# Kernel optimization log

Measured on AMD Instinct MI355X. Metric: run time of the kernel, lower is better.

## Reference

```python
import jax, jax.numpy as jnp
import numpy as np

N_NODES = 50000
E_EDGES = 800000
NEG_SLOPE = 0.2  # PyG GATConv LeakyReLU slope
BN_EPS = 1e-5


def _gat(x, src, dst, W, a_s, a_d, b, heads, ch, concat):
    """One GATConv (PyG semantics, eval mode): gather, per-edge attention,
    segment softmax over destination neighborhoods, scatter-add aggregation."""
    n = x.shape[0]
    h = (x @ W).reshape(n, heads, ch)                      # [N,H,C]
    es = jnp.sum(h * a_s, axis=-1)                         # [N,H] alpha_src per node
    ed = jnp.sum(h * a_d, axis=-1)                         # [N,H] alpha_dst per node
    e = jax.nn.leaky_relu(es[src] + ed[dst], NEG_SLOPE)    # [E,H] edge logits
    m = jax.ops.segment_max(e, dst, num_segments=n)        # stable segment softmax
    ex = jnp.exp(e - m[dst])
    den = jax.ops.segment_sum(ex, dst, num_segments=n)
    alpha = ex / den[dst]                                  # [E,H]
    out = jax.ops.segment_sum(h[src] * alpha[:, :, None], dst, num_segments=n)  # [N,H,C]
    out = out.reshape(n, heads * ch) if concat else out.mean(axis=1)
    return out + b


def _bn(x, g, b):
    # eval-mode BatchNorm1d with running_mean=0, running_var=1
    return x * (g / jnp.sqrt(1.0 + BN_EPS)) + b


def setup_inputs() -> dict:
    key = jax.random.key(0)
    k = jax.random.split(key, 24)
    s = 0.1
    inp = {
        "x": jax.random.normal(k[0], (N_NODES, 9), jnp.float32),
        "edge_index": jax.random.randint(k[1], (2, E_EDGES), 0, N_NODES, jnp.int32),
        "W1": jax.random.normal(k[2], (9, 512), jnp.float32) * s,
        "a1s": jax.random.normal(k[3], (8, 64), jnp.float32) * s,
        "a1d": jax.random.normal(k[4], (8, 64), jnp.float32) * s,
        "b1": jax.random.normal(k[5], (512,), jnp.float32) * s,
        "W2": jax.random.normal(k[6], (512, 128), jnp.float32) * s,
        "a2s": jax.random.normal(k[7], (4, 32), jnp.float32) * s,
        "a2d": jax.random.normal(k[8], (4, 32), jnp.float32) * s,
        "b2": jax.random.normal(k[9], (128,), jnp.float32) * s,
        "W3": jax.random.normal(k[10], (128, 32), jnp.float32) * s,
        "a3s": jax.random.normal(k[11], (1, 32), jnp.float32) * s,
        "a3d": jax.random.normal(k[12], (1, 32), jnp.float32) * s,
        "b3": jax.random.normal(k[13], (32,), jnp.float32) * s,
        "g1": jax.random.uniform(k[14], (512,), jnp.float32, 0.5, 1.5),
        "be1": jax.random.normal(k[15], (512,), jnp.float32) * s,
        "g2": jax.random.uniform(k[16], (128,), jnp.float32, 0.5, 1.5),
        "be2": jax.random.normal(k[17], (128,), jnp.float32) * s,
        "g3": jax.random.uniform(k[18], (32,), jnp.float32, 0.5, 1.5),
        "be3": jax.random.normal(k[19], (32,), jnp.float32) * s,
        "Wh": jax.random.normal(k[20], (32, 1), jnp.float32) * s,
        "bh": jax.random.normal(k[21], (1,), jnp.float32) * s,
    }
    return inp


def reference(x, edge_index, W1, a1s, a1d, b1, W2, a2s, a2d, b2,
              W3, a3s, a3d, b3, g1, be1, g2, be2, g3, be3, Wh, bh):
    n = x.shape[0]
    loops = jnp.arange(n, dtype=edge_index.dtype)          # PyG add_self_loops=True
    src = jnp.concatenate([edge_index[0], loops])
    dst = jnp.concatenate([edge_index[1], loops])
    h = _gat(x, src, dst, W1, a1s, a1d, b1, heads=8, ch=64, concat=True)
    h = jax.nn.elu(_bn(h, g1, be1))
    h = _gat(h, src, dst, W2, a2s, a2d, b2, heads=4, ch=32, concat=True)
    h = jax.nn.elu(_bn(h, g2, be2))
    h = _gat(h, src, dst, W3, a3s, a3d, b3, heads=1, ch=32, concat=False)
    h = jax.nn.elu(_bn(h, g3, be3))
    return h @ Wh + bh                                     # [N,1]
```

## Files before the change

### kernel.cpp

```cpp
#include <hip/hip_runtime.h>
#include <hip/hip_bf16.h>
#include <math.h>

#define N_NODES 50000
#define E_EDGES 800000
#define ET (E_EDGES + N_NODES)
#define NBLK_SCAN ((N_NODES + 255) / 256)
#define MPAD 50048
#define NPB_T1 16

typedef __attribute__((ext_vector_type(8))) short bf16x8;
typedef __attribute__((ext_vector_type(4))) float f32x4;


__global__ void zero_int_kernel(int* __restrict__ p, int n) {
    int i = blockIdx.x * blockDim.x + threadIdx.x;
    if (i < n) p[i] = 0;
}

__global__ void hist_kernel(const int* __restrict__ ei, int* __restrict__ cnt) {
    int e = blockIdx.x * blockDim.x + threadIdx.x;
    if (e < ET) {
        int d = (e < E_EDGES) ? ei[E_EDGES + e] : (e - E_EDGES);
        atomicAdd(&cnt[d], 1);
    }
}

__global__ void scan1_kernel(const int* __restrict__ cnt, int* __restrict__ rp,
                             int* __restrict__ bsum) {
    __shared__ int s[256];
    int i = blockIdx.x * 256 + threadIdx.x;
    int v = (i < N_NODES) ? cnt[i] : 0;
    s[threadIdx.x] = v;
    __syncthreads();
    for (int off = 1; off < 256; off <<= 1) {
        int t = (threadIdx.x >= off) ? s[threadIdx.x - off] : 0;
        __syncthreads();
        s[threadIdx.x] += t;
        __syncthreads();
    }
    if (i < N_NODES) rp[i + 1] = s[threadIdx.x];
    if (threadIdx.x == 255) bsum[blockIdx.x] = s[255];
}

__global__ void scan2_kernel(int* __restrict__ bsum, int nb) {
    __shared__ int s[256];
    int v = (threadIdx.x < nb) ? bsum[threadIdx.x] : 0;
    s[threadIdx.x] = v;
    __syncthreads();
    for (int off = 1; off < 256; off <<= 1) {
        int t = (threadIdx.x >= off) ? s[threadIdx.x - off] : 0;
        __syncthreads();
        s[threadIdx.x] += t;
        __syncthreads();
    }
    if (threadIdx.x < nb) bsum[threadIdx.x] = (threadIdx.x == 0) ? 0 : s[threadIdx.x - 1];
}

__global__ void scan3_kernel(int* __restrict__ rp, const int* __restrict__ bsum,
                             int* __restrict__ cursor) {
    int i = blockIdx.x * 256 + threadIdx.x;
    if (i == 0) rp[0] = 0;
    if (i < N_NODES) {
        int incl = rp[i + 1] + bsum[i >> 8];
        rp[i + 1] = incl;
        cursor[i] = incl - cursor[i];
    }
}

__global__ void fill_kernel(const int* __restrict__ ei, int* __restrict__ cursor,
                            int* __restrict__ col) {
    int e = blockIdx.x * blockDim.x + threadIdx.x;
    if (e < ET) {
        int s_, d;
        if (e < E_EDGES) { s_ = ei[e]; d = ei[E_EDGES + e]; }
        else             { s_ = e - E_EDGES; d = s_; }
        int p = atomicAdd(&cursor[d], 1);
        col[p] = s_;
    }
}


__global__ void prep_attn1_kernel(const float* __restrict__ W1,
                                  const float* __restrict__ a1s,
                                  const float* __restrict__ a1d,
                                  float* __restrict__ M) {
    int t = threadIdx.x;
    if (t < 144) {
        int which = t / 72, idx = t % 72, k = idx / 8, h = idx % 8;
        const float* a = which ? a1d : a1s;
        float s = 0.f;
        for (int c = 0; c < 64; c++) s += W1[k * 512 + h * 64 + c] * a[h * 64 + c];
        M[t] = s;
    }
}

__global__ void es_ed1_kernel(const float* __restrict__ x, const float* __restrict__ M,
                              float* __restrict__ es, float* __restrict__ ed) {
    int n = blockIdx.x * blockDim.x + threadIdx.x;
    if (n >= N_NODES) return;
    float xr[9];
#pragma unroll
    for (int k = 0; k < 9; k++) xr[k] = x[(size_t)n * 9 + k];
#pragma unroll
    for (int h = 0; h < 8; h++) {
        float s1 = 0.f, s2 = 0.f;
#pragma unroll
        for (int k = 0; k < 9; k++) {
            s1 += xr[k] * M[k * 8 + h];
            s2 += xr[k] * M[72 + k * 8 + h];
        }
        es[(size_t)n * 8 + h] = s1;
        ed[(size_t)n * 8 + h] = s2;
    }
}

__global__ __launch_bounds__(128) void agg1_kernel(const float* __restrict__ x,
        const int* __restrict__ rp, const int* __restrict__ col,
        const float* __restrict__ es, const float* __restrict__ ed,
        float* __restrict__ aggx) {
    __shared__ int   s_src[64];
    __shared__ float s_x[64][9];
    __shared__ float s_es[64][8];
    __shared__ float s_w[8][64];
    __shared__ float s_m[8], s_den[8], s_scale[8], s_ed[8];
    int n = blockIdx.x, tid = threadIdx.x;
    int start = rp[n], end = rp[n + 1];
    if (tid < 8) { s_m[tid] = -INFINITY; s_den[tid] = 0.f; s_ed[tid] = ed[(size_t)n * 8 + tid]; }
    __syncthreads();
    float acc = 0.f;
    int ghh = tid >> 4, glane = tid & 15;
    for (int cs = start; cs < end; cs += 64) {
        int cnt = min(64, end - cs);
        if (tid < cnt) s_src[tid] = col[cs + tid];
        __syncthreads();
        for (int q = tid; q < cnt * 9; q += 128) {
            int e = q / 9, k = q - e * 9;
            s_x[e][k] = x[(size_t)s_src[e] * 9 + k];
        }
        for (int q = tid; q < cnt * 8; q += 128) {
            int e = q >> 3, h = q & 7;
            s_es[e][h] = es[(size_t)s_src[e] * 8 + h];
        }
        __syncthreads();
        float lmax = -INFINITY;
        for (int e = glane; e < cnt; e += 16) {
            float l = s_es[e][ghh] + s_ed[ghh];
            l = (l > 0.f) ? l : 0.2f * l;
            s_w[ghh][e] = l;
            lmax = fmaxf(lmax, l);
        }
#pragma unroll
        for (int off = 8; off > 0; off >>= 1) lmax = fmaxf(lmax, __shfl_xor(lmax, off));
        float mold = s_m[ghh];
        float nm = fmaxf(mold, lmax);
        float fac = __expf(mold - nm);
        float psum = 0.f;
        for (int e = glane; e < cnt; e += 16) {
            float w = __expf(s_w[ghh][e] - nm);
            s_w[ghh][e] = w;
            psum += w;
        }
#pragma unroll
        for (int off = 8; off > 0; off >>= 1) psum += __shfl_xor(psum, off);
        if (glane == 0) { s_den[ghh] = s_den[ghh] * fac + psum; s_m[ghh] = nm; s_scale[ghh] = fac; }
        __syncthreads();
        if (tid < 72) {
            int hh = tid / 9, k = tid - hh * 9;
            float a = acc * s_scale[hh];
            for (int e = 0; e < cnt; e++) a += s_w[hh][e] * s_x[e][k];
            acc = a;
        }
        __syncthreads();
    }
    if (tid < 72) {
        int hh = tid / 9;
        aggx[(size_t)n * 72 + tid] = acc / s_den[hh];
    }
}

__global__ __launch_bounds__(256) void transform1_kernel(const float* __restrict__ aggx,
        const float* __restrict__ W1, const float* __restrict__ b1,
        const float* __restrict__ g1, const float* __restrict__ be1,
        __hip_bfloat16* __restrict__ Ah, __hip_bfloat16* __restrict__ Al) {
    __shared__ float s_a[NPB_T1 * 72];
    int tid = threadIdx.x;
    int n0 = blockIdx.x * NPB_T1;
    int nn = min(NPB_T1, N_NODES - n0);
    for (int q = tid; q < nn * 72; q += 256) s_a[q] = aggx[(size_t)n0 * 72 + q];
    int c0 = tid * 2;
    int hh = c0 >> 6;
    float2 wv[9];
#pragma unroll
    for (int k = 0; k < 9; k++) wv[k] = *(const float2*)&W1[k * 512 + c0];
    float2 bv = *(const float2*)&b1[c0];
    float2 gv = *(const float2*)&g1[c0];
    float2 ev = *(const float2*)&be1[c0];
    float gs0 = gv.x / sqrtf(1.00001f), gs1 = gv.y / sqrtf(1.00001f);
    __syncthreads();
    for (int i = 0; i < nn; i++) {
        const float* ar = &s_a[i * 72 + hh * 9];
        float v0 = bv.x, v1 = bv.y;
#pragma unroll
        for (int k = 0; k < 9; k++) { float a = ar[k]; v0 += a * wv[k].x; v1 += a * wv[k].y; }
        v0 = v0 * gs0 + ev.x;
        v1 = v1 * gs1 + ev.y;
        v0 = (v0 > 0.f) ? v0 : expm1f(v0);
        v1 = (v1 > 0.f) ? v1 : expm1f(v1);
        __hip_bfloat16 h0 = __float2bfloat16(v0), h1 = __float2bfloat16(v1);
        float r0 = v0 - __bfloat162float(h0), r1 = v1 - __bfloat162float(h1);
        size_t base = (size_t)(n0 + i) * 512 + c0;
        __hip_bfloat162 hp; hp.x = h0; hp.y = h1;
        __hip_bfloat162 lp; lp.x = __float2bfloat16(r0); lp.y = __float2bfloat16(r1);
        *(__hip_bfloat162*)&Ah[base] = hp;
        *(__hip_bfloat162*)&Al[base] = lp;
    }
}

__global__ void prep_w2_kernel(const float* __restrict__ W2,
                               __hip_bfloat16* __restrict__ Wh,
                               __hip_bfloat16* __restrict__ Wl) {
    int t = blockIdx.x * 256 + threadIdx.x;
    if (t < 512 * 128) {
        int k = t >> 7, c = t & 127;
        float v = W2[t];
        __hip_bfloat16 hi = __float2bfloat16(v);
        float r = v - __bfloat162float(hi);
        Wh[c * 512 + k] = hi;
        Wl[c * 512 + k] = __float2bfloat16(r);
    }
}


__global__ __launch_bounds__(256) void gemm2_mfma_kernel(
        const __hip_bfloat16* __restrict__ Ah, const __hip_bfloat16* __restrict__ Al,
        const __hip_bfloat16* __restrict__ Wh, const __hip_bfloat16* __restrict__ Wl,
        float* __restrict__ C) {
    __shared__ short lds[32768];
    int tid = threadIdx.x;
    int wv = tid >> 6;
    int lane = tid & 63;
    int lrow = lane & 15, kgrp = lane >> 4;
    int m0 = blockIdx.x * 128;

    f32x4 acc[2][8];
#pragma unroll
    for (int m = 0; m < 2; m++)
#pragma unroll
        for (int n = 0; n < 8; n++) acc[m][n] = (f32x4){0.f, 0.f, 0.f, 0.f};

    for (int kk = 0; kk < 512; kk += 64) {
#pragma unroll
        for (int tI = 0; tI < 4; tI++) {
            const __hip_bfloat16* src = (tI == 0) ? Ah : (tI == 1) ? Al : (tI == 2) ? Wh : Wl;
            int rowBase = (tI < 2) ? m0 : 0;
#pragma unroll
            for (int i = 0; i < 4; i++) {
                int gid = tid + 256 * i;
                int row = gid >> 3, kg = gid & 7;
                bf16x8 v = *(const bf16x8*)(src + (size_t)(rowBase + row) * 512 + kk + kg * 8);
                *(bf16x8*)(lds + tI * 8192 + row * 64 + ((kg ^ (row & 7)) << 3)) = v;
            }
        }
        __syncthreads();
#pragma unroll
        for (int ks = 0; ks < 2; ks++) {
            bf16x8 ah[2], al[2];
#pragma unroll
            for (int m = 0; m < 2; m++) {
                int row = wv * 32 + m * 16 + lrow;
                int kg = ks * 4 + kgrp;
                int so = row * 64 + ((kg ^ (row & 7)) << 3);
                ah[m] = *(const bf16x8*)(lds + so);
                al[m] = *(const bf16x8*)(lds + 8192 + so);
            }
#pragma unroll
            for (int n = 0; n < 8; n++) {
                int colr = n * 16 + lrow;
                int kg = ks * 4 + kgrp;
                int so = colr * 64 + ((kg ^ (colr & 7)) << 3);
                bf16x8 wh = *(const bf16x8*)(lds + 16384 + so);
                bf16x8 wl = *(const bf16x8*)(lds + 24576 + so);
#pragma unroll
                for (int m = 0; m < 2; m++) {
                    acc[m][n] = __builtin_amdgcn_mfma_f32_16x16x32_bf16(ah[m], wh, acc[m][n], 0, 0, 0);
                    acc[m][n] = __builtin_amdgcn_mfma_f32_16x16x32_bf16(al[m], wh, acc[m][n], 0, 0, 0);
                    acc[m][n] = __builtin_amdgcn_mfma_f32_16x16x32_bf16(ah[m], wl, acc[m][n], 0, 0, 0);
                }
            }
        }
        __syncthreads();
    }
#pragma unroll
    for (int m = 0; m < 2; m++) {
#pragma unroll
        for (int n = 0; n < 8; n++) {
#pragma unroll
            for (int r = 0; r < 4; r++) {
                int row = m0 + wv * 32 + m * 16 + (lane >> 4) * 4 + r;
                int colc = n * 16 + (lane & 15);
                if (row < N_NODES) C[(size_t)row * 128 + colc] = acc[m][n][r];
            }
        }
    }
}


template <int TN>
__global__ __launch_bounds__(256) void gemm_kernel(
        const float* __restrict__ A, const float* __restrict__ B,
        float* __restrict__ C, int M, int K, int Nd) {
    constexpr int BM = 64, BK = 16;
    constexpr int BN = 32 * TN;
    __shared__ float As[BM * BK];
    __shared__ float Bs[BK * BN];
    int tid = threadIdx.x;
    int m0 = blockIdx.x * BM;
    int n0 = blockIdx.y * BN;
    int tc = tid & 31;
    int tr = tid >> 5;
    float acc[8][TN];
#pragma unroll
    for (int i = 0; i < 8; i++)
#pragma unroll
        for (int j = 0; j < TN; j++) acc[i][j] = 0.f;

    for (int kk = 0; kk < K; kk += BK) {
#pragma unroll
        for (int l = 0; l < (BM * BK) / 256; l++) {
            int e = tid + 256 * l;
            int r = e >> 4, k = e & 15;
            float v = 0.f;
            if (m0 + r < M && kk + k < K) v = A[(size_t)(m0 + r) * K + kk + k];
            As[e] = v;
        }
#pragma unroll
        for (int l = 0; l < (BK * BN) / 256; l++) {
            int e = tid + 256 * l;
            int r = e / BN, c = e % BN;
            float v = 0.f;
            if (kk + r < K) v = B[(size_t)(kk + r) * Nd + n0 + c];
            Bs[e] = v;
        }
        __syncthreads();
#pragma unroll
        for (int k = 0; k < BK; k++) {
            float bv[TN];
#pragma unroll
            for (int j = 0; j < TN; j++) bv[j] = Bs[k * BN + tc * TN + j];
#pragma unroll
            for (int i = 0; i < 8; i++) {
                float a = As[(tr * 8 + i) * BK + k];
#pragma unroll
                for (int j = 0; j < TN; j++) acc[i][j] += a * bv[j];
            }
        }
        __syncthreads();
    }
#pragma unroll
    for (int i = 0; i < 8; i++) {
        int r = m0 + tr * 8 + i;
        if (r < M) {
#pragma unroll
            for (int j = 0; j < TN; j++)
                C[(size_t)r * Nd + n0 + tc * TN + j] = acc[i][j];
        }
    }
}


template <int H, int C>
__global__ void attn_dots_kernel(const float* __restrict__ hin,
                                 const float* __restrict__ as_, const float* __restrict__ ad_,
                                 float* __restrict__ es, float* __restrict__ ed) {
    int t = blockIdx.x * blockDim.x + threadIdx.x;
    if (t >= N_NODES * H) return;
    int n = t / H, hh = t % H;
    const float* row = hin + (size_t)n * (H * C) + hh * C;
    float s1 = 0.f, s2 = 0.f;
    for (int c = 0; c < C; c++) {
        float v = row[c];
        s1 += v * as_[hh * C + c];
        s2 += v * ad_[hh * C + c];
    }
    es[t] = s1;
    ed[t] = s2;
}


template <int H, int C>
__global__ __launch_bounds__((H * C < 64) ? 64 : H * C) void gat_agg_kernel(
        const float* __restrict__ hin,
        const int* __restrict__ rp, const int* __restrict__ col,
        const float* __restrict__ es, const float* __restrict__ ed,
        const float* __restrict__ bias, const float* __restrict__ gg,
        const float* __restrict__ bb,
        float* __restrict__ out) {
    constexpr int HC  = H * C;
    constexpr int BLK = (HC < 64) ? 64 : HC;
    constexpr int LPH = (BLK / H > 64) ? 64 : (BLK / H);
    constexpr int RT  = HC / 4;
    constexpr int G   = BLK / RT;
    constexpr int CH  = 64;
    __shared__ int   s_src[CH];
    __shared__ float s_w[H][CH];
    __shared__ float s_red[G][HC];
    __shared__ float s_m[H], s_den[H], s_scale[H], s_ed[H];

    int n = blockIdx.x;
    int tid = threadIdx.x;
    int start = rp[n], end = rp[n + 1];
    if (tid < H) {
        s_m[tid] = -INFINITY;
        s_den[tid] = 0.f;
        s_ed[tid] = ed[(size_t)n * H + tid];
    }
    __syncthreads();

    int ghh = tid / LPH, glane = tid % LPH;
    int g = tid / RT, rl = tid % RT;
    int hh2 = (rl * 4) / C;
    float ax = 0.f, ay = 0.f, az = 0.f, aw = 0.f;

    for (int cs = start; cs < end; cs += CH) {
        int cnt = min(CH, end - cs);
        if (tid < cnt) s_src[tid] = col[cs + tid];
        __syncthreads();

        {
            float lmax = -INFINITY;
            for (int e = glane; e < cnt; e += LPH) {
                float l = es[(size_t)s_src[e] * H + ghh] + s_ed[ghh];
                l = (l > 0.f) ? l : 0.2f * l;
                s_w[ghh][e] = l;
                lmax = fmaxf(lmax, l);
            }
#pragma unroll
            for (int off = LPH >> 1; off > 0; off >>= 1)
                lmax = fmaxf(lmax, __shfl_xor(lmax, off));
            float mold = s_m[ghh];
            float nm = fmaxf(mold, lmax);
            float fac = __expf(mold - nm);
            float psum = 0.f;
            for (int e = glane; e < cnt; e += LPH) {
                float w = __expf(s_w[ghh][e] - nm);
                s_w[ghh][e] = w;
                psum += w;
            }
#pragma unroll
            for (int off = LPH >> 1; off > 0; off >>= 1)
                psum += __shfl_xor(psum, off);
            if (glane == 0) {
                s_den[ghh] = s_den[ghh] * fac + psum;
                s_m[ghh] = nm;
                s_scale[ghh] = fac;
            }
        }
        __syncthreads();

        {
            float fac = s_scale[hh2];
            float bx = ax * fac, by = ay * fac, bz = az * fac, bw = aw * fac;
            float cx = 0.f, cy = 0.f, cz = 0.f, cw = 0.f;
            int e = g;
            for (; e + G < cnt; e += 2 * G) {
                float w0 = s_w[hh2][e];
                float w1 = s_w[hh2][e + G];
                float4 v0 = *(const float4*)&hin[(size_t)s_src[e] * HC + rl * 4];
                float4 v1 = *(const float4*)&hin[(size_t)s_src[e + G] * HC + rl * 4];
                bx += w0 * v0.x; by += w0 * v0.y; bz += w0 * v0.z; bw += w0 * v0.w;
                cx += w1 * v1.x; cy += w1 * v1.y; cz += w1 * v1.z; cw += w1 * v1.w;
            }
            if (e < cnt) {
                float w0 = s_w[hh2][e];
                float4 v0 = *(const float4*)&hin[(size_t)s_src[e] * HC + rl * 4];
                bx += w0 * v0.x; by += w0 * v0.y; bz += w0 * v0.z; bw += w0 * v0.w;
            }
            ax = bx + cx; ay = by + cy; az = bz + cz; aw = bw + cw;
        }
        __syncthreads();
    }

    s_red[g][rl * 4 + 0] = ax;
    s_red[g][rl * 4 + 1] = ay;
    s_red[g][rl * 4 + 2] = az;
    s_red[g][rl * 4 + 3] = aw;
    __syncthreads();
    if (tid < HC) {
        int hh = tid / C;
        float res = 0.f;
#pragma unroll
        for (int q = 0; q < G; q++) res += s_red[q][tid];
        res /= s_den[hh];
        res += bias[tid];
        res = res * (gg[tid] / sqrtf(1.00001f)) + bb[tid];
        res = (res > 0.f) ? res : expm1f(res);
        out[(size_t)n * HC + tid] = res;
    }
}


__global__ void head_kernel(const float* __restrict__ h3, const float* __restrict__ Wh,
                            const float* __restrict__ bh, float* __restrict__ out) {
    int n = blockIdx.x * blockDim.x + threadIdx.x;
    if (n < N_NODES) {
        float s = bh[0];
        const float* row = h3 + (size_t)n * 32;
#pragma unroll
        for (int c = 0; c < 32; c++) s += row[c] * Wh[c];
        out[n] = s;
    }
}


extern "C" void kernel_launch(void* const* d_in, const int* in_sizes, int n_in,
                              void* d_out, int out_size, void* d_ws, size_t ws_size,
                              hipStream_t stream) {
    const float* x   = (const float*)d_in[0];
    const int*   ei  = (const int*)d_in[1];
    const float* W1  = (const float*)d_in[2];
    const float* a1s = (const float*)d_in[3];
    const float* a1d = (const float*)d_in[4];
    const float* b1  = (const float*)d_in[5];
    const float* W2  = (const float*)d_in[6];
    const float* a2s = (const float*)d_in[7];
    const float* a2d = (const float*)d_in[8];
    const float* b2  = (const float*)d_in[9];
    const float* W3  = (const float*)d_in[10];
    const float* a3s = (const float*)d_in[11];
    const float* a3d = (const float*)d_in[12];
    const float* b3  = (const float*)d_in[13];
    const float* g1  = (const float*)d_in[14];
    const float* be1 = (const float*)d_in[15];
    const float* g2  = (const float*)d_in[16];
    const float* be2 = (const float*)d_in[17];
    const float* g3  = (const float*)d_in[18];
    const float* be3 = (const float*)d_in[19];
    const float* Wh  = (const float*)d_in[20];
    const float* bh  = (const float*)d_in[21];
    float* out = (float*)d_out;

    char* ws = (char*)d_ws;
    size_t off = 0;
    auto alloc = [&](size_t bytes) -> void* {
        void* p = ws + off;
        off += (bytes + 255) & ~(size_t)255;
        return p;
    };
    int*   row_ptr = (int*)alloc((N_NODES + 1) * sizeof(int));
    int*   cursor  = (int*)alloc((N_NODES + 1) * sizeof(int));
    int*   bsum    = (int*)alloc(256 * sizeof(int));
    int*   col_src = (int*)alloc((size_t)ET * sizeof(int));
    float* es      = (float*)alloc((size_t)N_NODES * 8 * sizeof(float));
    float* ed      = (float*)alloc((size_t)N_NODES * 8 * sizeof(float));
    float* bufA    = (float*)alloc((size_t)N_NODES * 128 * sizeof(float));
    float* bufB    = (float*)alloc((size_t)N_NODES * 128 * sizeof(float));
    float* bufC    = (float*)alloc((size_t)N_NODES * 32 * sizeof(float));
    __hip_bfloat16* Ah   = (__hip_bfloat16*)alloc((size_t)MPAD * 512 * sizeof(__hip_bfloat16));
    __hip_bfloat16* Al   = (__hip_bfloat16*)alloc((size_t)MPAD * 512 * sizeof(__hip_bfloat16));
    __hip_bfloat16* W2Th = (__hip_bfloat16*)alloc((size_t)128 * 512 * sizeof(__hip_bfloat16));
    __hip_bfloat16* W2Tl = (__hip_bfloat16*)alloc((size_t)128 * 512 * sizeof(__hip_bfloat16));
    float* M1 = (float*)(ws + ((ws_size - 1024) & ~(size_t)255));
    float* aggx = bufA;

    zero_int_kernel<<<(N_NODES + 1 + 255) / 256, 256, 0, stream>>>(cursor, N_NODES + 1);
    hist_kernel<<<(ET + 255) / 256, 256, 0, stream>>>(ei, cursor);
    scan1_kernel<<<NBLK_SCAN, 256, 0, stream>>>(cursor, row_ptr, bsum);
    scan2_kernel<<<1, 256, 0, stream>>>(bsum, NBLK_SCAN);
    scan3_kernel<<<NBLK_SCAN, 256, 0, stream>>>(row_ptr, bsum, cursor);
    fill_kernel<<<(ET + 255) / 256, 256, 0, stream>>>(ei, cursor, col_src);

    prep_attn1_kernel<<<1, 256, 0, stream>>>(W1, a1s, a1d, M1);
    es_ed1_kernel<<<(N_NODES + 255) / 256, 256, 0, stream>>>(x, M1, es, ed);
    agg1_kernel<<<N_NODES, 128, 0, stream>>>(x, row_ptr, col_src, es, ed, aggx);
    transform1_kernel<<<(N_NODES + NPB_T1 - 1) / NPB_T1, 256, 0, stream>>>(aggx, W1, b1, g1, be1, Ah, Al);

    prep_w2_kernel<<<256, 256, 0, stream>>>(W2, W2Th, W2Tl);
    gemm2_mfma_kernel<<<MPAD / 128, 256, 0, stream>>>(Ah, Al, W2Th, W2Tl, bufA);
    attn_dots_kernel<4, 32><<<(N_NODES * 4 + 255) / 256, 256, 0, stream>>>(bufA, a2s, a2d, es, ed);
    gat_agg_kernel<4, 32><<<N_NODES, 128, 0, stream>>>(bufA, row_ptr, col_src, es, ed,
                                                       b2, g2, be2, bufB);

    gemm_kernel<1><<<dim3((N_NODES + 63) / 64, 1), 256, 0, stream>>>(bufB, W3, bufC, N_NODES, 128, 32);
    attn_dots_kernel<1, 32><<<(N_NODES + 255) / 256, 256, 0, stream>>>(bufC, a3s, a3d, es, ed);
    gat_agg_kernel<1, 32><<<N_NODES, 64, 0, stream>>>(bufC, row_ptr, col_src, es, ed,
                                                      b3, g3, be3, bufA);

    head_kernel<<<(N_NODES + 255) / 256, 256, 0, stream>>>(bufA, Wh, bh, out);
}
```

Before: 457.4 us.

## Store layer 2 and 3 node features in fp16 to halve gather traffic

Result: faster. 431.8 us (-5.6%).

```diff
diff --git a/kernel.cpp b/kernel.cpp
--- a/kernel.cpp
+++ b/kernel.cpp
@@ -11,6 +11,7 @@
 
 typedef __attribute__((ext_vector_type(8))) short bf16x8;
 typedef __attribute__((ext_vector_type(4))) float f32x4;
+typedef __attribute__((ext_vector_type(8))) _Float16 half8;
 
 
 __global__ void zero_int_kernel(int* __restrict__ p, int n) {
@@ -235,7 +236,7 @@
 __global__ __launch_bounds__(256) void gemm2_mfma_kernel(
         const __hip_bfloat16* __restrict__ Ah, const __hip_bfloat16* __restrict__ Al,
         const __hip_bfloat16* __restrict__ Wh, const __hip_bfloat16* __restrict__ Wl,
-        float* __restrict__ C) {
+        _Float16* __restrict__ C) {
     __shared__ short lds[32768];
     int tid = threadIdx.x;
     int wv = tid >> 6;
@@ -299,7 +300,7 @@
             for (int r = 0; r < 4; r++) {
                 int row = m0 + wv * 32 + m * 16 + (lane >> 4) * 4 + r;
                 int colc = n * 16 + (lane & 15);
-                if (row < N_NODES) C[(size_t)row * 128 + colc] = acc[m][n][r];
+                if (row < N_NODES) C[(size_t)row * 128 + colc] = (_Float16)acc[m][n][r];
             }
         }
     }
@@ -307,9 +308,9 @@
 
 
 template <int TN>
-__global__ __launch_bounds__(256) void gemm_kernel(
+__global__ __launch_bounds__(256) void gemm_h_kernel(
         const float* __restrict__ A, const float* __restrict__ B,
-        float* __restrict__ C, int M, int K, int Nd) {
+        _Float16* __restrict__ C, int M, int K, int Nd) {
     constexpr int BM = 64, BK = 16;
     constexpr int BN = 32 * TN;
     __shared__ float As[BM * BK];
@@ -363,25 +364,30 @@
         if (r < M) {
 #pragma unroll
             for (int j = 0; j < TN; j++)
-                C[(size_t)r * Nd + n0 + tc * TN + j] = acc[i][j];
+                C[(size_t)r * Nd + n0 + tc * TN + j] = (_Float16)acc[i][j];
         }
     }
 }
 
 
 template <int H, int C>
-__global__ void attn_dots_kernel(const float* __restrict__ hin,
-                                 const float* __restrict__ as_, const float* __restrict__ ad_,
-                                 float* __restrict__ es, float* __restrict__ ed) {
+__global__ void attn_dots_h_kernel(const _Float16* __restrict__ hin,
+                                   const float* __restrict__ as_, const float* __restrict__ ad_,
+                                   float* __restrict__ es, float* __restrict__ ed) {
     int t = blockIdx.x * blockDim.x + threadIdx.x;
     if (t >= N_NODES * H) return;
     int n = t / H, hh = t % H;
-    const float* row = hin + (size_t)n * (H * C) + hh * C;
+    const half8* row = (const half8*)(hin + (size_t)n * (H * C) + hh * C);
     float s1 = 0.f, s2 = 0.f;
-    for (int c = 0; c < C; c++) {
-        float v = row[c];
-        s1 += v * as_[hh * C + c];
-        s2 += v * ad_[hh * C + c];
+#pragma unroll
+    for (int c8 = 0; c8 < C / 8; c8++) {
+        half8 v = row[c8];
+#pragma unroll
+        for (int j = 0; j < 8; j++) {
+            float f = (float)v[j];
+            s1 += f * as_[hh * C + c8 * 8 + j];
+            s2 += f * ad_[hh * C + c8 * 8 + j];
+        }
     }
     es[t] = s1;
     ed[t] = s2;
@@ -389,8 +395,8 @@
 
 
 template <int H, int C>
-__global__ __launch_bounds__((H * C < 64) ? 64 : H * C) void gat_agg_kernel(
-        const float* __restrict__ hin,
+__global__ __launch_bounds__((H * C < 64) ? 64 : H * C) void gat_agg_h_kernel(
+        const _Float16* __restrict__ hin,
         const int* __restrict__ rp, const int* __restrict__ col,
         const float* __restrict__ es, const float* __restrict__ ed,
         const float* __restrict__ bias, const float* __restrict__ gg,
@@ -399,7 +405,7 @@
     constexpr int HC  = H * C;
     constexpr int BLK = (HC < 64) ? 64 : HC;
     constexpr int LPH = (BLK / H > 64) ? 64 : (BLK / H);
-    constexpr int RT  = HC / 4;
+    constexpr int RT  = HC / 8;
     constexpr int G   = BLK / RT;
     constexpr int CH  = 64;
     __shared__ int   s_src[CH];
@@ -419,8 +425,10 @@
 
     int ghh = tid / LPH, glane = tid % LPH;
     int g = tid / RT, rl = tid % RT;
-    int hh2 = (rl * 4) / C;
-    float ax = 0.f, ay = 0.f, az = 0.f, aw = 0.f;
+    int hh2 = (rl * 8) / C;
+    float a0[8], a1[8];
+#pragma unroll
+    for (int j = 0; j < 8; j++) { a0[j] = 0.f; a1[j] = 0.f; }
 
     for (int cs = start; cs < end; cs += CH) {
         int cnt = min(CH, end - cs);
@@ -460,31 +468,31 @@
 
         {
             float fac = s_scale[hh2];
-            float bx = ax * fac, by = ay * fac, bz = az * fac, bw = aw * fac;
-            float cx = 0.f, cy = 0.f, cz = 0.f, cw = 0.f;
+#pragma unroll
+            for (int j = 0; j < 8; j++) a0[j] *= fac;
             int e = g;
             for (; e + G < cnt; e += 2 * G) {
                 float w0 = s_w[hh2][e];
                 float w1 = s_w[hh2][e + G];
-                float4 v0 = *(const float4*)&hin[(size_t)s_src[e] * HC + rl * 4];
-                float4 v1 = *(const float4*)&hin[(size_t)s_src[e + G] * HC + rl * 4];
-                bx += w0 * v0.x; by += w0 * v0.y; bz += w0 * v0.z; bw += w0 * v0.w;
-                cx += w1 * v1.x; cy += w1 * v1.y; cz += w1 * v1.z; cw += w1 * v1.w;
+                half8 v0 = *(const half8*)&hin[(size_t)s_src[e] * HC + rl * 8];
+                half8 v1 = *(const half8*)&hin[(size_t)s_src[e + G] * HC + rl * 8];
+#pragma unroll
+                for (int j = 0; j < 8; j++) a0[j] += w0 * (float)v0[j];
+#pragma unroll
+                for (int j = 0; j < 8; j++) a1[j] += w1 * (float)v1[j];
             }
             if (e < cnt) {
                 float w0 = s_w[hh2][e];
-                float4 v0 = *(const float4*)&hin[(size_t)s_src[e] * HC + rl * 4];
-                bx += w0 * v0.x; by += w0 * v0.y; bz += w0 * v0.z; bw += w0 * v0.w;
-            }
-            ax = bx + cx; ay = by + cy; az = bz + cz; aw = bw + cw;
-        }
-        __syncthreads();
-    }
-
-    s_red[g][rl * 4 + 0] = ax;
-    s_red[g][rl * 4 + 1] = ay;
-    s_red[g][rl * 4 + 2] = az;
-    s_red[g][rl * 4 + 3] = aw;
+                half8 v0 = *(const half8*)&hin[(size_t)s_src[e] * HC + rl * 8];
+#pragma unroll
+                for (int j = 0; j < 8; j++) a0[j] += w0 * (float)v0[j];
+            }
+        }
+        __syncthreads();
+    }
+
+#pragma unroll
+    for (int j = 0; j < 8; j++) s_red[g][rl * 8 + j] = a0[j] + a1[j];
     __syncthreads();
     if (tid < HC) {
         int hh = tid / C;
@@ -555,7 +563,8 @@
     float* ed      = (float*)alloc((size_t)N_NODES * 8 * sizeof(float));
     float* bufA    = (float*)alloc((size_t)N_NODES * 128 * sizeof(float));
     float* bufB    = (float*)alloc((size_t)N_NODES * 128 * sizeof(float));
-    float* bufC    = (float*)alloc((size_t)N_NODES * 32 * sizeof(float));
+    _Float16* h2h  = (_Float16*)alloc((size_t)N_NODES * 128 * sizeof(_Float16));
+    _Float16* h3h  = (_Float16*)alloc((size_t)N_NODES * 32 * sizeof(_Float16));
     __hip_bfloat16* Ah   = (__hip_bfloat16*)alloc((size_t)MPAD * 512 * sizeof(__hip_bfloat16));
     __hip_bfloat16* Al   = (__hip_bfloat16*)alloc((size_t)MPAD * 512 * sizeof(__hip_bfloat16));
     __hip_bfloat16* W2Th = (__hip_bfloat16*)alloc((size_t)128 * 512 * sizeof(__hip_bfloat16));
@@ -576,15 +585,15 @@
     transform1_kernel<<<(N_NODES + NPB_T1 - 1) / NPB_T1, 256, 0, stream>>>(aggx, W1, b1, g1, be1, Ah, Al);
 
     prep_w2_kernel<<<256, 256, 0, stream>>>(W2, W2Th, W2Tl);
-    gemm2_mfma_kernel<<<MPAD / 128, 256, 0, stream>>>(Ah, Al, W2Th, W2Tl, bufA);
-    attn_dots_kernel<4, 32><<<(N_NODES * 4 + 255) / 256, 256, 0, stream>>>(bufA, a2s, a2d, es, ed);
-    gat_agg_kernel<4, 32><<<N_NODES, 128, 0, stream>>>(bufA, row_ptr, col_src, es, ed,
-                                                       b2, g2, be2, bufB);
-
-    gemm_kernel<1><<<dim3((N_NODES + 63) / 64, 1), 256, 0, stream>>>(bufB, W3, bufC, N_NODES, 128, 32);
-    attn_dots_kernel<1, 32><<<(N_NODES + 255) / 256, 256, 0, stream>>>(bufC, a3s, a3d, es, ed);
-    gat_agg_kernel<1, 32><<<N_NODES, 64, 0, stream>>>(bufC, row_ptr, col_src, es, ed,
-                                                      b3, g3, be3, bufA);
+    gemm2_mfma_kernel<<<MPAD / 128, 256, 0, stream>>>(Ah, Al, W2Th, W2Tl, h2h);
+    attn_dots_h_kernel<4, 32><<<(N_NODES * 4 + 255) / 256, 256, 0, stream>>>(h2h, a2s, a2d, es, ed);
+    gat_agg_h_kernel<4, 32><<<N_NODES, 128, 0, stream>>>(h2h, row_ptr, col_src, es, ed,
+                                                         b2, g2, be2, bufB);
+
+    gemm_h_kernel<1><<<dim3((N_NODES + 63) / 64, 1), 256, 0, stream>>>(bufB, W3, h3h, N_NODES, 128, 32);
+    attn_dots_h_kernel<1, 32><<<(N_NODES + 255) / 256, 256, 0, stream>>>(h3h, a3s, a3d, es, ed);
+    gat_agg_h_kernel<1, 32><<<N_NODES, 64, 0, stream>>>(h3h, row_ptr, col_src, es, ed,
+                                                        b3, g3, be3, bufA);
 
     head_kernel<<<(N_NODES + 255) / 256, 256, 0, stream>>>(bufA, Wh, bh, out);
 }
```
